# Kernel tuning notes

Measured on AMD Instinct MI355X. Metric: run time of the kernel, lower is better.

## Reference

```python
import jax, jax.numpy as jnp
import numpy as np

DIM = 2048
HIDDEN = int(DIM * 2.6)  # 5324, matches int(dim*2.6) in torch
BATCH = 16384
EPS = 1e-12  # F.normalize default eps


def rmsnorm(x, g):
    # F.normalize(x, dim=-1) * dim**-0.5 * g
    n = jnp.linalg.norm(x, axis=-1, keepdims=True)
    return x / jnp.maximum(n, EPS) * (DIM ** -0.5) * g


def setup_inputs() -> dict:
    key = jax.random.key(0)
    ks = jax.random.split(key, 12)
    s = DIM ** -0.5
    return {
        "x": jax.random.normal(ks[0], (BATCH, DIM), jnp.float32),
        "state": jax.random.normal(ks[1], (BATCH, DIM), jnp.float32),
        "g1": jnp.ones((DIM,), jnp.float32),
        "g2": jnp.ones((DIM,), jnp.float32),
        "in_proj_w": jax.random.normal(ks[2], (3 * DIM, DIM), jnp.float32) * s,
        "in_proj_b": jnp.zeros((3 * DIM,), jnp.float32),
        "out_proj_w": jax.random.normal(ks[3], (DIM, DIM), jnp.float32) * s,
        "out_proj_b": jnp.zeros((DIM,), jnp.float32),
        "w1": jax.random.normal(ks[4], (HIDDEN, DIM), jnp.float32) * s,
        "w2": jax.random.normal(ks[5], (HIDDEN, DIM), jnp.float32) * s,
        "w3": jax.random.normal(ks[6], (DIM, HIDDEN), jnp.float32) * (HIDDEN ** -0.5),
    }


def reference(x, state, g1, g2, in_proj_w, in_proj_b, out_proj_w, out_proj_b, w1, w2, w3):
    h = x + state
    res = h
    hn = rmsnorm(h, g1)
    # MultiheadAttention with seq_len == 1: softmax over a single key is
    # exactly 1 for every head, so attn_out == out_proj(v_proj(hn)).
    wv = in_proj_w[2 * DIM:]
    bv = in_proj_b[2 * DIM:]
    v = hn @ wv.T + bv                      # [B, D]
    attn_out = v @ out_proj_w.T + out_proj_b
    h = res + attn_out
    hn2 = rmsnorm(h, g2)
    ffn = (jax.nn.silu(hn2 @ w1.T) * (hn2 @ w2.T)) @ w3.T
    return h + ffn
```

## Files before the change

### kernel.cpp

```cpp
#include <hip/hip_runtime.h>
#include <hip/hip_bf16.h>
#include <cstdint>
#include <cstddef>

#define DIMN   2048
#define BATCH  16384
#define HID    5324
#define HP     5376

typedef __bf16 bf16;
typedef __attribute__((ext_vector_type(8))) __bf16 bf16x8;
typedef __attribute__((ext_vector_type(4))) float floatx4;

#define GAS __attribute__((address_space(1)))
#define LAS __attribute__((address_space(3)))

__device__ __forceinline__ void async_copy16(const bf16* g, bf16* l) {
    __builtin_amdgcn_global_load_lds((const GAS uint32_t*)g, (LAS uint32_t*)l, 16, 0, 0);
}

template<int MODE>
__global__ __launch_bounds__(256, 2) void gemm_bt(
    const bf16* __restrict__ A, const bf16* __restrict__ W,
    const int K, const int N,
    const float* __restrict__ bias,
    float* __restrict__ f32io,
    bf16* __restrict__ bf16io)
{
    __shared__ __align__(16) bf16 ldsA[128 * 32];
    __shared__ __align__(16) bf16 ldsB[128 * 32];

    const int tid  = threadIdx.x;
    const int lane = tid & 63;
    const int wv   = tid >> 6;
    const int blockRow = blockIdx.y << 7;
    const int blockCol = blockIdx.x << 7;

    const int sRow = wv * 32 + (lane >> 2);
    const int sCol = (lane & 3) * 8;
    const bf16* gA0 = A + (size_t)(blockRow + sRow) * K + sCol;
    const bf16* gA1 = gA0 + (size_t)16 * K;
    const bf16* gB0 = W + (size_t)(blockCol + sRow) * K + sCol;
    const bf16* gB1 = gB0 + (size_t)16 * K;
    bf16* lA0 = &ldsA[wv * 1024];
    bf16* lA1 = lA0 + 512;
    bf16* lB0 = &ldsB[wv * 1024];
    bf16* lB1 = lB0 + 512;

    const int wm = wv >> 1, wn = wv & 1;
    const int m16 = lane & 15, quad = lane >> 4;
    const int aOff = (wm * 64 + m16) * 32 + quad * 8;
    const int bOff = (wn * 64 + m16) * 32 + quad * 8;

    floatx4 acc[4][4];
    const floatx4 zero = {0.f, 0.f, 0.f, 0.f};
#pragma unroll
    for (int i = 0; i < 4; i++)
#pragma unroll
        for (int j = 0; j < 4; j++) acc[i][j] = zero;

    const int kIters = K >> 5;
    for (int kk = 0; kk < kIters; ++kk) {
        async_copy16(gA0, lA0);
        async_copy16(gA1, lA1);
        async_copy16(gB0, lB0);
        async_copy16(gB1, lB1);
        gA0 += 32; gA1 += 32; gB0 += 32; gB1 += 32;
        __syncthreads();

        bf16x8 a[4], b[4];
#pragma unroll
        for (int i = 0; i < 4; i++) a[i] = *(const bf16x8*)&ldsA[aOff + i * 512];
#pragma unroll
        for (int j = 0; j < 4; j++) b[j] = *(const bf16x8*)&ldsB[bOff + j * 512];
#pragma unroll
        for (int i = 0; i < 4; i++)
#pragma unroll
            for (int j = 0; j < 4; j++)
                acc[i][j] = __builtin_amdgcn_mfma_f32_16x16x32_bf16(a[i], b[j], acc[i][j], 0, 0, 0);
        __syncthreads();
    }

#pragma unroll
    for (int j = 0; j < 4; j++) {
        const int col = blockCol + wn * 64 + j * 16 + m16;
        float bv = 0.f;
        if (MODE == 0 || MODE == 1) bv = bias[col];
#pragma unroll
        for (int i = 0; i < 4; i++) {
            const int row0 = blockRow + wm * 64 + i * 16 + quad * 4;
#pragma unroll
            for (int r = 0; r < 4; r++) {
                const size_t idx = (size_t)(row0 + r) * N + col;
                const float val = acc[i][j][r];
                if (MODE == 0) {
                    bf16io[idx] = (bf16)(val + bv);
                } else if (MODE == 1) {
                    f32io[idx] = f32io[idx] + val + bv;
                } else if (MODE == 2) {
                    bf16io[idx] = (bf16)(val / (1.f + __expf(-val)));
                } else if (MODE == 3) {
                    const float m = (float)bf16io[idx] * val;
                    bf16io[idx] = (bf16)m;
                } else {
                    f32io[idx] = f32io[idx] + val;
                }
            }
        }
    }
}

__global__ __launch_bounds__(256) void rms_add_kernel(
    const float* __restrict__ x, const float* __restrict__ st,
    const float* __restrict__ g, float* __restrict__ h, bf16* __restrict__ hn)
{
    const int row = blockIdx.x;
    const int tid = threadIdx.x;
    const float4* x4 = (const float4*)(x + (size_t)row * DIMN);
    const float4* s4 = (const float4*)(st + (size_t)row * DIMN);
    float4* h4 = (float4*)(h + (size_t)row * DIMN);
    const float4* g4 = (const float4*)g;

    float4 hv[2];
    float ss = 0.f;
#pragma unroll
    for (int c = 0; c < 2; c++) {
        const int i = tid + c * 256;
        const float4 a = x4[i];
        const float4 b = s4[i];
        float4 t;
        t.x = a.x + b.x; t.y = a.y + b.y; t.z = a.z + b.z; t.w = a.w + b.w;
        h4[i] = t;
        hv[c] = t;
        ss += t.x * t.x + t.y * t.y + t.z * t.z + t.w * t.w;
    }
#pragma unroll
    for (int off = 32; off; off >>= 1) ss += __shfl_xor(ss, off, 64);
    __shared__ float red[4];
    if ((tid & 63) == 0) red[tid >> 6] = ss;
    __syncthreads();
    const float tot = red[0] + red[1] + red[2] + red[3];
    const float scale = 0.02209708691207961f / fmaxf(sqrtf(tot), 1e-12f);

    bf16* o = hn + (size_t)row * DIMN;
#pragma unroll
    for (int c = 0; c < 2; c++) {
        const int i = tid + c * 256;
        const float4 gv = g4[i];
        const float4 t = hv[c];
        o[i * 4 + 0] = (bf16)(t.x * scale * gv.x);
        o[i * 4 + 1] = (bf16)(t.y * scale * gv.y);
        o[i * 4 + 2] = (bf16)(t.z * scale * gv.z);
        o[i * 4 + 3] = (bf16)(t.w * scale * gv.w);
    }
}

__global__ __launch_bounds__(256) void rms_kernel(
    const float* __restrict__ h, const float* __restrict__ g, bf16* __restrict__ hn)
{
    const int row = blockIdx.x;
    const int tid = threadIdx.x;
    const float4* h4 = (const float4*)(h + (size_t)row * DIMN);
    const float4* g4 = (const float4*)g;

    float4 hv[2];
    float ss = 0.f;
#pragma unroll
    for (int c = 0; c < 2; c++) {
        const int i = tid + c * 256;
        const float4 t = h4[i];
        hv[c] = t;
        ss += t.x * t.x + t.y * t.y + t.z * t.z + t.w * t.w;
    }
#pragma unroll
    for (int off = 32; off; off >>= 1) ss += __shfl_xor(ss, off, 64);
    __shared__ float red[4];
    if ((tid & 63) == 0) red[tid >> 6] = ss;
    __syncthreads();
    const float tot = red[0] + red[1] + red[2] + red[3];
    const float scale = 0.02209708691207961f / fmaxf(sqrtf(tot), 1e-12f);

    bf16* o = hn + (size_t)row * DIMN;
#pragma unroll
    for (int c = 0; c < 2; c++) {
        const int i = tid + c * 256;
        const float4 gv = g4[i];
        const float4 t = hv[c];
        o[i * 4 + 0] = (bf16)(t.x * scale * gv.x);
        o[i * 4 + 1] = (bf16)(t.y * scale * gv.y);
        o[i * 4 + 2] = (bf16)(t.z * scale * gv.z);
        o[i * 4 + 3] = (bf16)(t.w * scale * gv.w);
    }
}

__global__ __launch_bounds__(256) void cvt_pad_kernel(
    const float* __restrict__ src, bf16* __restrict__ dst,
    const int srcRows, const int srcCols, const int dstCols)
{
    const int col = blockIdx.x * 256 + threadIdx.x;
    const int row = blockIdx.y;
    if (col >= dstCols) return;
    float v = 0.f;
    if (row < srcRows && col < srcCols) v = src[(size_t)row * srcCols + col];
    dst[(size_t)row * dstCols + col] = (bf16)v;
}

extern "C" void kernel_launch(void* const* d_in, const int* in_sizes, int n_in,
                              void* d_out, int out_size, void* d_ws, size_t ws_size,
                              hipStream_t stream)
{
    const float* x   = (const float*)d_in[0];
    const float* st  = (const float*)d_in[1];
    const float* g1  = (const float*)d_in[2];
    const float* g2  = (const float*)d_in[3];
    const float* ipw = (const float*)d_in[4];
    const float* ipb = (const float*)d_in[5];
    const float* opw = (const float*)d_in[6];
    const float* opb = (const float*)d_in[7];
    const float* w1  = (const float*)d_in[8];
    const float* w2  = (const float*)d_in[9];
    const float* w3  = (const float*)d_in[10];
    float* out = (float*)d_out;

    char* wsb = (char*)d_ws;
    bf16* hn  = (bf16*)(wsb + 0);
    bf16* vb  = (bf16*)(wsb + 67108864);
    bf16* sa  = (bf16*)(wsb + 134217728);
    bf16* wvb = (bf16*)(wsb + 310378496);
    bf16* wob = (bf16*)(wsb + 318767104);
    bf16* w1b = (bf16*)(wsb + 327155712);
    bf16* w2b = (bf16*)(wsb + 349175808);
    bf16* w3b = (bf16*)(wsb + 371195904);

    cvt_pad_kernel<<<dim3(8, 2048), 256, 0, stream>>>(ipw + (size_t)2 * DIMN * DIMN, wvb, 2048, 2048, 2048);
    cvt_pad_kernel<<<dim3(8, 2048), 256, 0, stream>>>(opw, wob, 2048, 2048, 2048);
    cvt_pad_kernel<<<dim3(8, HP),   256, 0, stream>>>(w1, w1b, HID, 2048, 2048);
    cvt_pad_kernel<<<dim3(8, HP),   256, 0, stream>>>(w2, w2b, HID, 2048, 2048);
    cvt_pad_kernel<<<dim3(21, 2048),256, 0, stream>>>(w3, w3b, 2048, HID, HP);

    rms_add_kernel<<<BATCH, 256, 0, stream>>>(x, st, g1, out, hn);

    gemm_bt<0><<<dim3(16, 128), 256, 0, stream>>>(hn, wvb, 2048, 2048, ipb + 2 * DIMN, nullptr, vb);

    gemm_bt<1><<<dim3(16, 128), 256, 0, stream>>>(vb, wob, 2048, 2048, opb, out, nullptr);

    rms_kernel<<<BATCH, 256, 0, stream>>>(out, g2, hn);

    gemm_bt<2><<<dim3(42, 128), 256, 0, stream>>>(hn, w1b, 2048, HP, nullptr, nullptr, sa);

    gemm_bt<3><<<dim3(42, 128), 256, 0, stream>>>(hn, w2b, 2048, HP, nullptr, nullptr, sa);

    gemm_bt<4><<<dim3(16, 128), 256, 0, stream>>>(sa, w3b, HP, 2048, nullptr, out, nullptr);
}
```

Measured before the change: 2.622 ms.

## Rewrite GEMM with 256x256 tiles, triple-buffered async LDS pipeline and swizzle

Each GEMM block now computes a 256x256 tile with 8 waves and keeps three K-stage LDS buffers, so async global-to-LDS loads for stage t+2 overlap the MFMAs on stage t. The barrier-per-iteration pattern is replaced with explicit vmcnt waits. The change also adds an XOR swizzle on LDS addresses to avoid bank conflicts, an XCD-aware block remapping, and setprio around the MFMA bursts. The aim is to raise arithmetic intensity and hide memory latency. In exchange it uses far more LDS and registers per block, which lowers occupancy, and the larger tiles give fewer blocks for the smaller GEMMs.

```diff
diff --git a/kernel.cpp b/kernel.cpp
--- a/kernel.cpp
+++ b/kernel.cpp
@@ -20,65 +20,112 @@
 }
 
 template<int MODE>
-__global__ __launch_bounds__(256, 2) void gemm_bt(
+__global__ __launch_bounds__(512, 2) void gemm_bt(
     const bf16* __restrict__ A, const bf16* __restrict__ W,
     const int K, const int N,
     const float* __restrict__ bias,
     float* __restrict__ f32io,
     bf16* __restrict__ bf16io)
 {
-    __shared__ __align__(16) bf16 ldsA[128 * 32];
-    __shared__ __align__(16) bf16 ldsB[128 * 32];
+    __shared__ __align__(16) bf16 lds[49152];
 
     const int tid  = threadIdx.x;
     const int lane = tid & 63;
     const int wv   = tid >> 6;
-    const int blockRow = blockIdx.y << 7;
-    const int blockCol = blockIdx.x << 7;
-
-    const int sRow = wv * 32 + (lane >> 2);
-    const int sCol = (lane & 3) * 8;
-    const bf16* gA0 = A + (size_t)(blockRow + sRow) * K + sCol;
-    const bf16* gA1 = gA0 + (size_t)16 * K;
-    const bf16* gB0 = W + (size_t)(blockCol + sRow) * K + sCol;
-    const bf16* gB1 = gB0 + (size_t)16 * K;
-    bf16* lA0 = &ldsA[wv * 1024];
-    bf16* lA1 = lA0 + 512;
-    bf16* lB0 = &ldsB[wv * 1024];
-    bf16* lB1 = lB0 + 512;
-
-    const int wm = wv >> 1, wn = wv & 1;
+    const int wm   = wv >> 2;
+    const int wn   = wv & 3;
+
+    const int gx  = gridDim.x;
+    const int nwg = gx * gridDim.y;
+    int lin = blockIdx.y * gx + blockIdx.x;
+    if ((nwg & 7) == 0) lin = (lin & 7) * (nwg >> 3) + (lin >> 3);
+    const int bx = lin % gx, by = lin / gx;
+    const int blockRow = by << 8;
+    const int blockCol = bx << 8;
+
+    const int sg = ((lane & 3) ^ ((lane >> 3) & 3)) * 8;
+    const bf16* pA[2];
+    const bf16* pB[2];
+#pragma unroll
+    for (int i = 0; i < 2; i++) {
+        pA[i] = A + (size_t)(blockRow + i * 128 + wv * 16 + (lane >> 2)) * K + sg;
+        pB[i] = W + (size_t)(blockCol + i * 128 + wv * 16 + (lane >> 2)) * K + sg;
+    }
+
     const int m16 = lane & 15, quad = lane >> 4;
-    const int aOff = (wm * 64 + m16) * 32 + quad * 8;
-    const int bOff = (wn * 64 + m16) * 32 + quad * 8;
-
-    floatx4 acc[4][4];
+    const int rg = (quad ^ ((m16 >> 1) & 3)) * 8;
+    const int aBase = (wm * 128 + m16) * 32 + rg;
+    const int bBase = 8192 + (wn * 64 + m16) * 32 + rg;
+
+    floatx4 acc[8][4];
     const floatx4 zero = {0.f, 0.f, 0.f, 0.f};
 #pragma unroll
-    for (int i = 0; i < 4; i++)
+    for (int i = 0; i < 8; i++)
 #pragma unroll
         for (int j = 0; j < 4; j++) acc[i][j] = zero;
 
-    const int kIters = K >> 5;
-    for (int kk = 0; kk < kIters; ++kk) {
-        async_copy16(gA0, lA0);
-        async_copy16(gA1, lA1);
-        async_copy16(gB0, lB0);
-        async_copy16(gB1, lB1);
-        gA0 += 32; gA1 += 32; gB0 += 32; gB1 += 32;
-        __syncthreads();
-
-        bf16x8 a[4], b[4];
-#pragma unroll
-        for (int i = 0; i < 4; i++) a[i] = *(const bf16x8*)&ldsA[aOff + i * 512];
-#pragma unroll
-        for (int j = 0; j < 4; j++) b[j] = *(const bf16x8*)&ldsB[bOff + j * 512];
+    const int nt = K >> 5;
+
+#pragma unroll
+    for (int i = 0; i < 2; i++) {
+        async_copy16(pA[i], &lds[i * 4096 + wv * 512]);
+        async_copy16(pB[i], &lds[8192 + i * 4096 + wv * 512]);
+    }
+#pragma unroll
+    for (int i = 0; i < 2; i++) { pA[i] += 32; pB[i] += 32; }
+#pragma unroll
+    for (int i = 0; i < 2; i++) {
+        async_copy16(pA[i], &lds[16384 + i * 4096 + wv * 512]);
+        async_copy16(pB[i], &lds[16384 + 8192 + i * 4096 + wv * 512]);
+    }
+#pragma unroll
+    for (int i = 0; i < 2; i++) { pA[i] += 32; pB[i] += 32; }
+    asm volatile("s_waitcnt vmcnt(4)" ::: "memory");
+    __builtin_amdgcn_s_barrier();
+
+    int sCur = 0, sNxt = 32768;
+    for (int t = 0; t < nt; ++t) {
+        const bool pf = (t + 2) < nt;
+
+        if (pf) {
+            async_copy16(pA[0], &lds[sNxt + wv * 512]);
+            async_copy16(pA[1], &lds[sNxt + 4096 + wv * 512]);
+        }
+        bf16x8 bfr[4], afr[4];
+#pragma unroll
+        for (int j = 0; j < 4; j++) bfr[j] = *(const bf16x8*)&lds[sCur + bBase + j * 512];
+#pragma unroll
+        for (int i = 0; i < 4; i++) afr[i] = *(const bf16x8*)&lds[sCur + aBase + i * 512];
+        __builtin_amdgcn_s_setprio(1);
 #pragma unroll
         for (int i = 0; i < 4; i++)
 #pragma unroll
             for (int j = 0; j < 4; j++)
-                acc[i][j] = __builtin_amdgcn_mfma_f32_16x16x32_bf16(a[i], b[j], acc[i][j], 0, 0, 0);
-        __syncthreads();
+                acc[i][j] = __builtin_amdgcn_mfma_f32_16x16x32_bf16(afr[i], bfr[j], acc[i][j], 0, 0, 0);
+        __builtin_amdgcn_s_setprio(0);
+        __builtin_amdgcn_s_barrier();
+
+        if (pf) {
+            async_copy16(pB[0], &lds[sNxt + 8192 + wv * 512]);
+            async_copy16(pB[1], &lds[sNxt + 8192 + 4096 + wv * 512]);
+            pA[0] += 32; pA[1] += 32; pB[0] += 32; pB[1] += 32;
+        }
+#pragma unroll
+        for (int i = 0; i < 4; i++) afr[i] = *(const bf16x8*)&lds[sCur + aBase + 2048 + i * 512];
+        __builtin_amdgcn_s_setprio(1);
+#pragma unroll
+        for (int i = 0; i < 4; i++)
+#pragma unroll
+            for (int j = 0; j < 4; j++)
+                acc[i + 4][j] = __builtin_amdgcn_mfma_f32_16x16x32_bf16(afr[i], bfr[j], acc[i + 4][j], 0, 0, 0);
+        __builtin_amdgcn_s_setprio(0);
+
+        if (pf) { asm volatile("s_waitcnt vmcnt(4)" ::: "memory"); }
+        else    { asm volatile("s_waitcnt vmcnt(0)" ::: "memory"); }
+        __builtin_amdgcn_s_barrier();
+
+        sCur = (sCur == 32768) ? 0 : sCur + 16384;
+        sNxt = (sNxt == 32768) ? 0 : sNxt + 16384;
     }
 
 #pragma unroll
@@ -87,8 +134,8 @@
         float bv = 0.f;
         if (MODE == 0 || MODE == 1) bv = bias[col];
 #pragma unroll
-        for (int i = 0; i < 4; i++) {
-            const int row0 = blockRow + wm * 64 + i * 16 + quad * 4;
+        for (int i = 0; i < 8; i++) {
+            const int row0 = blockRow + wm * 128 + i * 16 + quad * 4;
 #pragma unroll
             for (int r = 0; r < 4; r++) {
                 const size_t idx = (size_t)(row0 + r) * N + col;
@@ -240,15 +287,15 @@
 
     rms_add_kernel<<<BATCH, 256, 0, stream>>>(x, st, g1, out, hn);
 
-    gemm_bt<0><<<dim3(16, 128), 256, 0, stream>>>(hn, wvb, 2048, 2048, ipb + 2 * DIMN, nullptr, vb);
-
-    gemm_bt<1><<<dim3(16, 128), 256, 0, stream>>>(vb, wob, 2048, 2048, opb, out, nullptr);
+    gemm_bt<0><<<dim3(8, 64), 512, 0, stream>>>(hn, wvb, 2048, 2048, ipb + 2 * DIMN, nullptr, vb);
+
+    gemm_bt<1><<<dim3(8, 64), 512, 0, stream>>>(vb, wob, 2048, 2048, opb, out, nullptr);
 
     rms_kernel<<<BATCH, 256, 0, stream>>>(out, g2, hn);
 
-    gemm_bt<2><<<dim3(42, 128), 256, 0, stream>>>(hn, w1b, 2048, HP, nullptr, nullptr, sa);
-
-    gemm_bt<3><<<dim3(42, 128), 256, 0, stream>>>(hn, w2b, 2048, HP, nullptr, nullptr, sa);
-
-    gemm_bt<4><<<dim3(16, 128), 256, 0, stream>>>(sa, w3b, HP, 2048, nullptr, out, nullptr);
-}
+    gemm_bt<2><<<dim3(21, 64), 512, 0, stream>>>(hn, w1b, 2048, HP, nullptr, nullptr, sa);
+
+    gemm_bt<3><<<dim3(21, 64), 512, 0, stream>>>(hn, w2b, 2048, HP, nullptr, nullptr, sa);
+
+    gemm_bt<4><<<dim3(8, 64), 512, 0, stream>>>(sa, w3b, HP, 2048, nullptr, out, nullptr);
+}
```

After: 2.210 ms. 15.7% less time.
